# Kernel tuning notes

Hardware: AMD Instinct MI355X
Metric: run time of the kernel (lower is better)

Reference implementation:

```python
import jax, jax.numpy as jnp
import numpy as np

B, N, D, H = 8, 512, 512, 8
DK = D // H          # 64
DIM_G = 64           # trigonometric geometry embedding dim
WAVE_LEN = 1000.0


def box_relational_embedding(f_g):
    # f_g: [B, N, 4] -> [B, N, N, 64]
    x_min, y_min, x_max, y_max = [f_g[..., i] for i in range(4)]  # [B,N]
    cx = (x_min + x_max) * 0.5
    cy = (y_min + y_max) * 0.5
    w = x_max - x_min + 1.0
    h = y_max - y_min + 1.0
    # pairwise deltas; divide by w_i / h_i of the row box (broadcast over j)
    dx = jnp.log(jnp.clip(jnp.abs((cx[:, :, None] - cx[:, None, :]) / w[:, :, None]), 0.001))
    dy = jnp.log(jnp.clip(jnp.abs((cy[:, :, None] - cy[:, None, :]) / h[:, :, None]), 0.001))
    dw = jnp.log(w[:, :, None] / w[:, None, :])
    dh = jnp.log(h[:, :, None] / h[:, None, :])
    pos = jnp.stack([dx, dy, dw, dh], axis=-1)  # [B,N,N,4]
    feat_range = jnp.arange(DIM_G // 8, dtype=jnp.float32) / (DIM_G / 8.0)  # [8]
    dim_mat = 1.0 / (WAVE_LEN ** feat_range)  # [8]
    mul = (100.0 * pos)[..., None] * dim_mat  # [B,N,N,4,8]
    mul = mul.reshape(pos.shape[0], pos.shape[1], pos.shape[2], -1)  # [B,N,N,32]
    return jnp.concatenate([jnp.sin(mul), jnp.cos(mul)], axis=-1)  # [B,N,N,64]


def setup_inputs() -> dict:
    key = jax.random.key(0)
    ks = jax.random.split(key, 12)
    s = 1.0 / np.sqrt(D)
    return {
        "input_query": jax.random.normal(ks[0], (B, N, D), jnp.float32),
        "input_key": jax.random.normal(ks[1], (B, N, D), jnp.float32),
        "input_value": jax.random.normal(ks[2], (B, N, D), jnp.float32),
        "input_box": jax.random.uniform(ks[3], (B, N, 4), jnp.float32),
        "mask": jax.random.randint(ks[4], (B, N), 0, 2, jnp.int32),
        "not_objects": jax.random.randint(ks[5], (B, N), 0, 2).astype(jnp.bool_),
        "Wq": jax.random.normal(ks[6], (D, D), jnp.float32) * s,
        "bq": jnp.zeros((D,), jnp.float32),
        "Wk": jax.random.normal(ks[7], (D, D), jnp.float32) * s,
        "bk": jnp.zeros((D,), jnp.float32),
        "Wv": jax.random.normal(ks[8], (D, D), jnp.float32) * s,
        "bv": jnp.zeros((D,), jnp.float32),
        "Wo": jax.random.normal(ks[9], (D, D), jnp.float32) * s,
        "bo": jnp.zeros((D,), jnp.float32),
        "WG": jax.random.normal(ks[10], (H, DIM_G), jnp.float32) * 0.1,
        "bG": jnp.zeros((H,), jnp.float32),
    }


def reference(input_query, input_key, input_value, input_box, mask, not_objects,
              Wq, bq, Wk, bk, Wv, bv, Wo, bo, WG, bG):
    emb = box_relational_embedding(input_box)  # [B,N,N,64]

    def proj(x, W, b):
        return (x @ W + b).reshape(B, N, H, DK).transpose(0, 2, 1, 3)  # [B,H,N,DK]

    q = proj(input_query, Wq, bq)
    k = proj(input_key, Wk, bk)
    v = proj(input_value, Wv, bv)

    scores = jnp.einsum('bhnd,bhmd->bhnm', q, k) / np.sqrt(DK).astype(np.float32)
    scores = jnp.where(mask[:, None, None, :] == 0, -1e9, scores)

    # per-head geometry weights: [B,H,N,N]
    wg = jax.nn.relu(jnp.einsum('bnmg,hg->bhnm', emb, WG) + bG[None, :, None, None])

    # object mask: zero the geometry log-bias where either i or j is not an object
    pair_not_obj = not_objects[:, None, :, None] | not_objects[:, None, None, :]  # [B,1,N,N]
    mask_obj = 1.0 - pair_not_obj.astype(jnp.float32)

    logits = jnp.log(jnp.clip(wg, 1e-6)) * mask_obj + scores
    attn = jax.nn.softmax(logits, axis=-1)  # dropout is identity in eval mode

    out = jnp.einsum('bhnm,bhmd->bhnd', attn, v)
    out = out.transpose(0, 2, 1, 3).reshape(B, N, D)
    return out @ Wo + bo
```

## Files before the change

### kernel.cpp

```cpp
#include <hip/hip_runtime.h>
#include <hip/hip_fp16.h>

#define B_ 8
#define N_ 512
#define D_ 512
#define H_ 8
#define DK_ 64

typedef unsigned int uint;
typedef unsigned short ushort;
typedef __attribute__((ext_vector_type(8))) short short8;
typedef __attribute__((ext_vector_type(8))) _Float16 half8;
typedef __attribute__((ext_vector_type(4))) float floatx4;

__device__ __forceinline__ float bf2f(ushort s) { return __uint_as_float(((uint)s) << 16); }
__device__ __forceinline__ ushort f2bf(float f) {
    uint x = __float_as_uint(f);
    return (ushort)((x + 0x7fffu + ((x >> 16) & 1u)) >> 16);
}
__device__ __forceinline__ float blo(uint u) { return __uint_as_float(u << 16); }
__device__ __forceinline__ float bhi(uint u) { return __uint_as_float(u & 0xffff0000u); }
__device__ __forceinline__ float ldf(const void* p, size_t i, int isbf) {
    return isbf ? bf2f(((const ushort*)p)[i]) : ((const float*)p)[i];
}
__device__ __forceinline__ short ldb(const void* p, size_t i, int isbf) {
    return isbf ? (short)(((const ushort*)p)[i]) : (short)f2bf(((const float*)p)[i]);
}

__global__ __launch_bounds__(256) void probe_dtype(const uint* __restrict__ q,
                                                   int* __restrict__ flag) {
    __shared__ int s[256];
    const int t = threadIdx.x;
    int cnt = 0;
    for (int i = t; i < 4096; i += 256) {
        const uint e = (q[i] >> 7) & 0xffu;
        cnt += (e >= 0x70u && e <= 0x84u) ? 1 : 0;
    }
    s[t] = cnt;
    __syncthreads();
    for (int d = 128; d > 0; d >>= 1) {
        if (t < d) s[t] += s[t + d];
        __syncthreads();
    }
    if (t == 0) *flag = (s[0] > 3276) ? 1 : 0;
}

__global__ __launch_bounds__(256) void prep_bias(const void* __restrict__ b0,
                                                 const void* __restrict__ b1,
                                                 const void* __restrict__ b2,
                                                 const void* __restrict__ b3,
                                                 float* __restrict__ biasf,
                                                 const int* __restrict__ flagp) {
    const int isbf = *flagp;
    const int e = blockIdx.x * 256 + threadIdx.x;
    const int z = e >> 9;
    const void* src = (z == 0) ? b0 : (z == 1) ? b1 : (z == 2) ? b2 : b3;
    biasf[e] = ldf(src, e & 511, isbf);
}

__global__ __launch_bounds__(256) void transw(const void* __restrict__ w0,
                                              const void* __restrict__ w1,
                                              const void* __restrict__ w2,
                                              const void* __restrict__ w3,
                                              ushort* __restrict__ wt,
                                              const int* __restrict__ flagp) {
    const int isbf = *flagp;
    const int z = blockIdx.z;
    const void* W = (z == 0) ? w0 : (z == 1) ? w1 : (z == 2) ? w2 : w3;
    const int n0 = blockIdx.x * 32, k0 = blockIdx.y * 32;
    __shared__ float tile[32][33];
    const int tx = threadIdx.x & 31, ty = threadIdx.x >> 5;
#pragma unroll
    for (int r = 0; r < 4; ++r)
        tile[ty + 8 * r][tx] = ldf(W, (size_t)(k0 + ty + 8 * r) * D_ + n0 + tx, isbf);
    __syncthreads();
#pragma unroll
    for (int r = 0; r < 4; ++r)
        wt[(size_t)z * 262144 + (size_t)(n0 + ty + 8 * r) * D_ + k0 + tx] =
            f2bf(tile[tx][ty + 8 * r]);
}

template <typename AT, int MODE>
__global__ __launch_bounds__(256) void gemm_mfma(
    const AT* __restrict__ A0, const AT* __restrict__ A1, const AT* __restrict__ A2,
    const ushort* __restrict__ wt, const float* __restrict__ biasf,
    ushort* __restrict__ oq, ushort* __restrict__ ok, ushort* __restrict__ ov,
    void* __restrict__ dout, const int* __restrict__ flagp, int want) {
    if (want >= 0 && *flagp != want) return;
    const int z = (MODE == 0) ? blockIdx.z : 3;
    const AT* A = (MODE == 0) ? ((z == 0) ? A0 : (z == 1) ? A1 : A2) : A0;
    const ushort* W = wt + (size_t)z * 262144;
    const float* bias = biasf + z * 512;
    const int row0 = blockIdx.x * 128, col0 = blockIdx.y * 64;
    const int t = threadIdx.x, wv = t >> 6, lane = t & 63;
    const int m16 = lane & 15, quad = lane >> 4;

    __shared__ ushort As[128][40];
    __shared__ ushort Ws[64][40];
    floatx4 acc[2][4] = {};

    const int ar = t >> 1, ah = t & 1;
    const int wr = t >> 2, wc = (t & 3) * 8;

    for (int k0 = 0; k0 < D_; k0 += 32) {
        __syncthreads();
        {
            const AT* ap = A + (size_t)(row0 + ar) * D_ + k0 + ah * 16;
            short8 s0, s1;
            if constexpr (sizeof(AT) == 4) {
                const float4 f0 = *(const float4*)(ap);
                const float4 f1 = *(const float4*)(ap + 4);
                const float4 f2 = *(const float4*)(ap + 8);
                const float4 f3 = *(const float4*)(ap + 12);
                s0[0] = (short)f2bf(f0.x); s0[1] = (short)f2bf(f0.y);
                s0[2] = (short)f2bf(f0.z); s0[3] = (short)f2bf(f0.w);
                s0[4] = (short)f2bf(f1.x); s0[5] = (short)f2bf(f1.y);
                s0[6] = (short)f2bf(f1.z); s0[7] = (short)f2bf(f1.w);
                s1[0] = (short)f2bf(f2.x); s1[1] = (short)f2bf(f2.y);
                s1[2] = (short)f2bf(f2.z); s1[3] = (short)f2bf(f2.w);
                s1[4] = (short)f2bf(f3.x); s1[5] = (short)f2bf(f3.y);
                s1[6] = (short)f2bf(f3.z); s1[7] = (short)f2bf(f3.w);
            } else {
                s0 = *(const short8*)(ap);
                s1 = *(const short8*)(ap + 8);
            }
            *(short8*)&As[ar][ah * 16] = s0;
            *(short8*)&As[ar][ah * 16 + 8] = s1;
        }
        *(short8*)&Ws[wr][wc] =
            *(const short8*)(W + (size_t)(col0 + wr) * D_ + k0 + wc);
        __syncthreads();

        const short8 a0 = *(const short8*)&As[wv * 32 + m16][quad * 8];
        const short8 a1 = *(const short8*)&As[wv * 32 + 16 + m16][quad * 8];
        const short8 b0 = *(const short8*)&Ws[m16][quad * 8];
        const short8 b1 = *(const short8*)&Ws[16 + m16][quad * 8];
        const short8 b2 = *(const short8*)&Ws[32 + m16][quad * 8];
        const short8 b3 = *(const short8*)&Ws[48 + m16][quad * 8];
        acc[0][0] = __builtin_amdgcn_mfma_f32_16x16x32_bf16(a0, b0, acc[0][0], 0, 0, 0);
        acc[0][1] = __builtin_amdgcn_mfma_f32_16x16x32_bf16(a0, b1, acc[0][1], 0, 0, 0);
        acc[0][2] = __builtin_amdgcn_mfma_f32_16x16x32_bf16(a0, b2, acc[0][2], 0, 0, 0);
        acc[0][3] = __builtin_amdgcn_mfma_f32_16x16x32_bf16(a0, b3, acc[0][3], 0, 0, 0);
        acc[1][0] = __builtin_amdgcn_mfma_f32_16x16x32_bf16(a1, b0, acc[1][0], 0, 0, 0);
        acc[1][1] = __builtin_amdgcn_mfma_f32_16x16x32_bf16(a1, b1, acc[1][1], 0, 0, 0);
        acc[1][2] = __builtin_amdgcn_mfma_f32_16x16x32_bf16(a1, b2, acc[1][2], 0, 0, 0);
        acc[1][3] = __builtin_amdgcn_mfma_f32_16x16x32_bf16(a1, b3, acc[1][3], 0, 0, 0);
    }

    const int isbf = *flagp;
#pragma unroll
    for (int mt = 0; mt < 2; ++mt) {
#pragma unroll
        for (int nt = 0; nt < 4; ++nt) {
            const int colg = col0 + nt * 16 + m16;
            const float bi = bias[colg];
            float v0 = acc[mt][nt][0] + bi, v1 = acc[mt][nt][1] + bi;
            float v2 = acc[mt][nt][2] + bi, v3 = acc[mt][nt][3] + bi;
            const int rowb = row0 + wv * 32 + mt * 16 + quad * 4;
            if (MODE == 0) {
                if (z == 2) {
                    const int bhv = (rowb >> 9) * H_ + (colg >> 6);
                    uint2 pk;
                    pk.x = (uint)f2bf(v0) | ((uint)f2bf(v1) << 16);
                    pk.y = (uint)f2bf(v2) | ((uint)f2bf(v3) << 16);
                    *(uint2*)(ov + ((size_t)bhv * DK_ + (colg & 63)) * N_ + (rowb & 511)) = pk;
                } else {
                    ushort* o = (z == 0) ? oq : ok;
                    const float vv[4] = {v0, v1, v2, v3};
#pragma unroll
                    for (int r = 0; r < 4; ++r) {
                        const int row = rowb + r;
                        o[((size_t)((row >> 9) * H_ + (colg >> 6)) * N_ + (row & 511)) * DK_ +
                          (colg & 63)] = f2bf(vv[r]);
                    }
                }
            } else {
                const float vv[4] = {v0, v1, v2, v3};
#pragma unroll
                for (int r = 0; r < 4; ++r) {
                    const int row = rowb + r;
                    if (isbf) ((ushort*)dout)[(size_t)row * D_ + colg] = f2bf(vv[r]);
                    else      ((float*)dout)[(size_t)row * D_ + colg] = vv[r];
                }
            }
        }
    }
}

__global__ __launch_bounds__(256) void geom2(const void* __restrict__ box,
                                             const int* __restrict__ nobj,
                                             const void* __restrict__ WG,
                                             const void* __restrict__ bG,
                                             ushort* __restrict__ glog,
                                             const int* __restrict__ flagp) {
    const int isbf = *flagp;
    const int i = blockIdx.x, bl = blockIdx.y;
    const int t = threadIdx.x;

    __shared__ _Float16 trig[128][72];
    __shared__ _Float16 wgf[16][72];
    __shared__ float mobja[128];
    __shared__ float bgs[8];

    for (int e = t; e < 1024; e += 256) {
        const int h = e >> 6, g = e & 63;
        wgf[h][g] = (_Float16)((h < 8) ? ldf(WG, (size_t)h * 64 + g, isbf) : 0.f);
    }
    if (t < 8) bgs[t] = ldf(bG, t, isbf);

    const size_t ib = (size_t)(bl * N_ + i) * 4;
    const float ixn = ldf(box, ib + 0, isbf), iyn = ldf(box, ib + 1, isbf);
    const float ixx = ldf(box, ib + 2, isbf), iyx = ldf(box, ib + 3, isbf);
    const float wi = ixx - ixn + 1.0f, hi = iyx - iyn + 1.0f;
    const float cxi = (ixn + ixx) * 0.5f, cyi = (iyn + iyx) * 0.5f;
    const float rwi = 1.0f / wi, rhi = 1.0f / hi;
    const float lwi = __logf(wi), lhi = __logf(hi);
    const int noi = nobj[bl * N_ + i];
    __syncthreads();

    const int wv = t >> 6, lane = t & 63, m16 = lane & 15, quad = lane >> 4;
    const half8 bf0 = *(const half8*)&wgf[m16][quad * 8];
    const half8 bf1 = *(const half8*)&wgf[m16][quad * 8 + 32];
    _Float16* gb = (_Float16*)glog +
                   ((((size_t)bl * 32 + (i >> 4)) * 8) * 16 + (i & 15)) * 512;
    const float dm[8] = {1.0f, 0.421696503f, 0.177827941f, 0.074989421f,
                         0.031622777f, 0.013335214f, 0.005623413f, 0.002371374f};

    for (int c = 0; c < 4; ++c) {
        const int jbase = c * 128;
        {
            const int pair = t >> 1, hf = t & 1;
            const int j = jbase + pair;
            const size_t jb = (size_t)(bl * N_ + j) * 4;
            const float jxn = ldf(box, jb + 0, isbf), jyn = ldf(box, jb + 1, isbf);
            const float jxx = ldf(box, jb + 2, isbf), jyx = ldf(box, jb + 3, isbf);
            const float wj = jxx - jxn + 1.0f, hj = jyx - jyn + 1.0f;
            float p0, p1;
            if (hf == 0) {
                const float cxj = (jxn + jxx) * 0.5f, cyj = (jyn + jyx) * 0.5f;
                p0 = __logf(fmaxf(fabsf((cxi - cxj) * rwi), 0.001f));
                p1 = __logf(fmaxf(fabsf((cyi - cyj) * rhi), 0.001f));
                mobja[pair] = (noi || nobj[bl * N_ + j]) ? 0.f : 1.f;
            } else {
                p0 = lwi - __logf(wj);
                p1 = lhi - __logf(hj);
            }
#pragma unroll
            for (int pp = 0; pp < 2; ++pp) {
                const float base = 100.f * (pp ? p1 : p0);
                half8 s8, c8;
#pragma unroll
                for (int f = 0; f < 8; ++f) {
                    float sv, cv;
                    __sincosf(base * dm[f], &sv, &cv);
                    s8[f] = (_Float16)sv;
                    c8[f] = (_Float16)cv;
                }
                const int g0 = hf * 16 + pp * 8;
                *(half8*)&trig[pair][g0] = s8;
                *(half8*)&trig[pair][32 + g0] = c8;
            }
        }
        __syncthreads();
        {
#pragma unroll
            for (int sub = 0; sub < 2; ++sub) {
                const int pr0 = wv * 32 + sub * 16;
                const half8 a0 = *(const half8*)&trig[pr0 + m16][quad * 8];
                const half8 a1 = *(const half8*)&trig[pr0 + m16][quad * 8 + 32];
                floatx4 acc = {};
                acc = __builtin_amdgcn_mfma_f32_16x16x32_f16(a0, bf0, acc, 0, 0, 0);
                acc = __builtin_amdgcn_mfma_f32_16x16x32_f16(a1, bf1, acc, 0, 0, 0);
                if (m16 < 8) {
#pragma unroll
                    for (int r = 0; r < 4; ++r) {
                        const int pair = pr0 + quad * 4 + r;
                        const float wg = acc[r] + bgs[m16];
                        const float gl = __logf(fmaxf(wg, 1e-6f)) * mobja[pair];
                        gb[(size_t)m16 * 8192 + jbase + pair] = (_Float16)gl;
                    }
                }
            }
        }
        __syncthreads();
    }
}

__global__ __launch_bounds__(256) void attn3(
    const ushort* __restrict__ qw, const ushort* __restrict__ kw,
    const ushort* __restrict__ vt, const int* __restrict__ mask,
    const ushort* __restrict__ glog, ushort* __restrict__ att, int b0) {
    const int it = blockIdx.x, h = blockIdx.y, bl = blockIdx.z;
    const int bg = b0 + bl;
    const int i0 = it * 16;
    const int t = threadIdx.x, wv = t >> 6, lane = t & 63;
    const int m16 = lane & 15, quad = lane >> 4;
    const size_t bh = (size_t)(bg * H_ + h);

    __shared__ float lg[16][516];
    __shared__ ushort sbuf[16 * 520];
    __shared__ float rsumInv[16];

    {
        const uint4* src = (const uint4*)(glog + (((size_t)bl * 32 + it) * 8 + h) * 8192);
        uint4* dst = (uint4*)sbuf;
#pragma unroll
        for (int e = 0; e < 4; ++e) dst[t + 256 * e] = src[t + 256 * e];
    }
    const ushort* qrow = qw + (bh * N_ + i0 + m16) * DK_ + quad * 8;
    const short8 aq0 = *(const short8*)(qrow);
    const short8 aq1 = *(const short8*)(qrow + 32);
    __syncthreads();

#pragma unroll
    for (int tt = 0; tt < 8; ++tt) {
        const int j0 = wv * 128 + tt * 16;
        const ushort* krow = kw + (bh * N_ + j0 + m16) * DK_ + quad * 8;
        const short8 bk0 = *(const short8*)(krow);
        const short8 bk1 = *(const short8*)(krow + 32);
        floatx4 acc = {};
        acc = __builtin_amdgcn_mfma_f32_16x16x32_bf16(aq0, bk0, acc, 0, 0, 0);
        acc = __builtin_amdgcn_mfma_f32_16x16x32_bf16(aq1, bk1, acc, 0, 0, 0);
        const int mj = mask[bg * N_ + j0 + m16];
        const __half* gt = (const __half*)sbuf;
#pragma unroll
        for (int r = 0; r < 4; ++r) {
            const int i = quad * 4 + r;
            const float g = __half2float(gt[i * 512 + j0 + m16]);
            lg[i][j0 + m16] = (mj ? 0.125f * acc[r] : -1e9f) + g;
        }
    }
    __syncthreads();

    {
        const int row = t >> 4, l = t & 15;
        float v[32];
        float mx = -3e38f;
#pragma unroll
        for (int s = 0; s < 32; ++s) { v[s] = lg[row][l + 16 * s]; mx = fmaxf(mx, v[s]); }
#pragma unroll
        for (int d = 1; d < 16; d <<= 1) mx = fmaxf(mx, __shfl_xor(mx, d, 16));
        float sm = 0.f;
#pragma unroll
        for (int s = 0; s < 32; ++s) { const float p = __expf(v[s] - mx); sm += p; v[s] = p; }
#pragma unroll
        for (int d = 1; d < 16; d <<= 1) sm += __shfl_xor(sm, d, 16);
#pragma unroll
        for (int s = 0; s < 32; ++s) sbuf[row * 520 + l + 16 * s] = f2bf(v[s]);
        if (l == 0) rsumInv[row] = 1.0f / sm;
    }
    __syncthreads();

    {
        const int dk0 = wv * 16;
        const ushort* vrow = vt + (bh * DK_ + dk0 + m16) * N_ + quad * 8;
        floatx4 oc = {};
#pragma unroll
        for (int kc = 0; kc < 16; ++kc) {
            const short8 ap = *(const short8*)(sbuf + m16 * 520 + kc * 32 + quad * 8);
            const short8 bv = *(const short8*)(vrow + kc * 32);
            oc = __builtin_amdgcn_mfma_f32_16x16x32_bf16(ap, bv, oc, 0, 0, 0);
        }
#pragma unroll
        for (int r = 0; r < 4; ++r) {
            const int i = quad * 4 + r;
            const float o = oc[r] * rsumInv[i];
            att[((size_t)(bg * N_ + i0 + i)) * D_ + h * DK_ + dk0 + m16] = f2bf(o);
        }
    }
}

__global__ __launch_bounds__(256) void gemm16(const void* __restrict__ A,
                                              const void* __restrict__ W,
                                              const void* __restrict__ bias,
                                              void* __restrict__ out,
                                              const int* __restrict__ flagp,
                                              int a_follows, int mode) {
    const int isbf = *flagp;
    const int a_isbf = a_follows ? isbf : 1;
    const int wave = threadIdx.x >> 6;
    const int tile = blockIdx.x * 4 + wave;
    const int tm = tile >> 5, tn = tile & 31;
    const int row0 = tm * 16, col0 = tn * 16;
    const int lane = threadIdx.x & 63;
    const int m = lane & 15, quad = lane >> 4;
    floatx4 acc = {0.f, 0.f, 0.f, 0.f};
    const size_t abase = (size_t)(row0 + m) * D_ + quad * 8;
    const size_t wbase = (size_t)(quad * 8) * D_ + col0 + m;
    for (int k0 = 0; k0 < D_; k0 += 32) {
        short8 af, bf;
#pragma unroll
        for (int j = 0; j < 8; ++j) af[j] = ldb(A, abase + k0 + j, a_isbf);
#pragma unroll
        for (int j = 0; j < 8; ++j) bf[j] = ldb(W, wbase + (size_t)(k0 + j) * D_, isbf);
        acc = __builtin_amdgcn_mfma_f32_16x16x32_bf16(af, bf, acc, 0, 0, 0);
    }
    const int col = col0 + m;
    const float bi = ldf(bias, col, isbf);
#pragma unroll
    for (int r = 0; r < 4; ++r) {
        const int row = row0 + quad * 4 + r;
        const float v = acc[r] + bi;
        if (mode == 1) {
            ((ushort*)out)[(size_t)(((row >> 9) * H_ + (col >> 6)) * N_ + (row & 511)) * DK_ + (col & 63)] = f2bf(v);
        } else if (isbf) {
            ((ushort*)out)[(size_t)row * D_ + col] = f2bf(v);
        } else {
            ((float*)out)[(size_t)row * D_ + col] = v;
        }
    }
}

__global__ __launch_bounds__(256) void attn_old(
    const ushort* __restrict__ qw, const ushort* __restrict__ kw,
    const ushort* __restrict__ vw, const void* __restrict__ box,
    const int* __restrict__ mask, const int* __restrict__ nobj,
    const void* __restrict__ WG, const void* __restrict__ bG,
    ushort* __restrict__ att, const int* __restrict__ flagp) {
    const int isbf = *flagp;
    const int b = blockIdx.z, h = blockIdx.y;
    const int i0 = blockIdx.x * 8;
    const int t = threadIdx.x;
    __shared__ float lg[8][520];
    __shared__ float q_s[8][68];
    __shared__ float wgh[64];
    __shared__ float cxi[8], cyi[8], rwi[8], rhi[8], lwi[8], lhi[8];
    __shared__ int noi[8];
    __shared__ float rsum[8];
    for (int e = t; e < 512; e += 256) {
        const int ii = e >> 6, dk = e & 63;
        q_s[ii][dk] = bf2f(qw[(size_t)((b * H_ + h) * N_ + i0 + ii) * DK_ + dk]) * 0.125f;
    }
    if (t < 64) wgh[t] = ldf(WG, h * 64 + t, isbf);
    if (t < 8) {
        const size_t bb = (size_t)(b * N_ + i0 + t) * 4;
        const float xmn = ldf(box, bb + 0, isbf), ymn = ldf(box, bb + 1, isbf);
        const float xmx = ldf(box, bb + 2, isbf), ymx = ldf(box, bb + 3, isbf);
        const float w = xmx - xmn + 1.0f, hh = ymx - ymn + 1.0f;
        cxi[t] = (xmn + xmx) * 0.5f;
        cyi[t] = (ymn + ymx) * 0.5f;
        rwi[t] = 1.0f / w;
        rhi[t] = 1.0f / hh;
        lwi[t] = __logf(w);
        lhi[t] = __logf(hh);
        noi[t] = nobj[b * N_ + i0 + t];
    }
    const float bg = ldf(bG, h, isbf);
    __syncthreads();
    for (int jl = 0; jl < 2; ++jl) {
        const int j = t + jl * 256;
        float acc[8];
#pragma unroll
        for (int ii = 0; ii < 8; ++ii) acc[ii] = 0.f;
        const uint4* krow = (const uint4*)(kw + (size_t)((b * H_ + h) * N_ + j) * DK_);
#pragma unroll
        for (int c = 0; c < 8; ++c) {
            const uint4 ku = krow[c];
            float kf[8];
            kf[0] = blo(ku.x); kf[1] = bhi(ku.x); kf[2] = blo(ku.y); kf[3] = bhi(ku.y);
            kf[4] = blo(ku.z); kf[5] = bhi(ku.z); kf[6] = blo(ku.w); kf[7] = bhi(ku.w);
#pragma unroll
            for (int ii = 0; ii < 8; ++ii) {
                const float4 qa = *(const float4*)(&q_s[ii][c * 8]);
                const float4 qb = *(const float4*)(&q_s[ii][c * 8 + 4]);
                acc[ii] += qa.x * kf[0] + qa.y * kf[1] + qa.z * kf[2] + qa.w * kf[3] +
                           qb.x * kf[4] + qb.y * kf[5] + qb.z * kf[6] + qb.w * kf[7];
            }
        }
        const int mj = mask[b * N_ + j];
        const size_t bb = (size_t)(b * N_ + j) * 4;
        const float xmn = ldf(box, bb + 0, isbf), ymn = ldf(box, bb + 1, isbf);
        const float xmx = ldf(box, bb + 2, isbf), ymx = ldf(box, bb + 3, isbf);
        const float cxj = (xmn + xmx) * 0.5f, cyj = (ymn + ymx) * 0.5f;
        const float wj = xmx - xmn + 1.0f, hj = ymx - ymn + 1.0f;
        const float lwj = __logf(wj), lhj = __logf(hj);
        const int noj = nobj[b * N_ + j];
        const float dm[8] = {1.0f, 0.421696503f, 0.177827941f, 0.074989421f,
                             0.031622777f, 0.013335214f, 0.005623413f, 0.002371374f};
        for (int ii = 0; ii < 8; ++ii) {
            const float mobj = (noi[ii] || noj) ? 0.f : 1.f;
            const float dx = __logf(fmaxf(fabsf((cxi[ii] - cxj) * rwi[ii]), 0.001f));
            const float dy = __logf(fmaxf(fabsf((cyi[ii] - cyj) * rhi[ii]), 0.001f));
            const float pos[4] = {dx, dy, lwi[ii] - lwj, lhi[ii] - lhj};
            float wg = bg;
            for (int p = 0; p < 4; ++p) {
                const float base = 100.f * pos[p];
#pragma unroll
                for (int f = 0; f < 8; ++f) {
                    float sv, cv;
                    __sincosf(base * dm[f], &sv, &cv);
                    const int g = p * 8 + f;
                    wg += sv * wgh[g] + cv * wgh[32 + g];
                }
            }
            lg[ii][j] = (mj ? acc[ii] : -1e9f) + __logf(fmaxf(wg, 1e-6f)) * mobj;
        }
    }
    __syncthreads();
    {
        const int rr = t >> 5, l32 = t & 31;
        float mx = -3e38f;
        for (int j = l32; j < N_; j += 32) mx = fmaxf(mx, lg[rr][j]);
#pragma unroll
        for (int d = 1; d < 32; d <<= 1) mx = fmaxf(mx, __shfl_xor(mx, d, 32));
        float sm = 0.f;
        for (int j = l32; j < N_; j += 32) {
            const float p = __expf(lg[rr][j] - mx);
            lg[rr][j] = p;
            sm += p;
        }
#pragma unroll
        for (int d = 1; d < 32; d <<= 1) sm += __shfl_xor(sm, d, 32);
        if (l32 == 0) rsum[rr] = sm;
    }
    __syncthreads();
    {
        const int ii = t >> 5, dkp = t & 31;
        float o0 = 0.f, o1 = 0.f;
        const uint* vbase = (const uint*)vw + (size_t)((b * H_ + h) * N_) * (DK_ / 2) + dkp;
        for (int j = 0; j < N_; ++j) {
            const uint u = vbase[(size_t)j * (DK_ / 2)];
            const float p = lg[ii][j];
            o0 += p * blo(u);
            o1 += p * bhi(u);
        }
        const float inv = 1.0f / rsum[ii];
        const uint pk = (uint)f2bf(o0 * inv) | ((uint)f2bf(o1 * inv) << 16);
        ((uint*)att)[(size_t)(b * N_ + i0 + ii) * (D_ / 2) + h * 32 + dkp] = pk;
    }
}

extern "C" void kernel_launch(void* const* d_in, const int* in_sizes, int n_in,
                              void* d_out, int out_size, void* d_ws, size_t ws_size,
                              hipStream_t stream) {
    const void* xq = d_in[0];
    const void* xk = d_in[1];
    const void* xv = d_in[2];
    const void* box = d_in[3];
    const int* mask = (const int*)d_in[4];
    const int* nobj = (const int*)d_in[5];
    const void* Wq = d_in[6];
    const void* bq = d_in[7];
    const void* Wk = d_in[8];
    const void* bk = d_in[9];
    const void* Wv = d_in[10];
    const void* bv = d_in[11];
    const void* Wo = d_in[12];
    const void* bo = d_in[13];
    const void* WG = d_in[14];
    const void* bG = d_in[15];

    char* ws = (char*)d_ws;
    const size_t MB = 1u << 20;

    if (ws_size >= 54 * MB) {
        int* flag = (int*)ws;
        float* biasf = (float*)(ws + 4096);
        ushort* wt = (ushort*)(ws + 16384);
        size_t p = 16384 + 2097152;
        ushort* qw = (ushort*)(ws + p); p += 4194304;
        ushort* kw = (ushort*)(ws + p); p += 4194304;
        ushort* vt = (ushort*)(ws + p); p += 4194304;
        ushort* att = (ushort*)(ws + p); p += 4194304;
        ushort* glog = (ushort*)(ws + p);

        hipLaunchKernelGGL(probe_dtype, dim3(1), dim3(256), 0, stream, (const uint*)xq, flag);
        hipLaunchKernelGGL(prep_bias, dim3(8), dim3(256), 0, stream, bq, bk, bv, bo, biasf, flag);
        hipLaunchKernelGGL(transw, dim3(16, 16, 4), dim3(256), 0, stream, Wq, Wk, Wv, Wo, wt, flag);
        hipLaunchKernelGGL((gemm_mfma<float, 0>), dim3(32, 8, 3), dim3(256), 0, stream,
                           (const float*)xq, (const float*)xk, (const float*)xv,
                           wt, biasf, qw, kw, vt, (void*)nullptr, flag, 0);
        hipLaunchKernelGGL((gemm_mfma<ushort, 0>), dim3(32, 8, 3), dim3(256), 0, stream,
                           (const ushort*)xq, (const ushort*)xk, (const ushort*)xv,
                           wt, biasf, qw, kw, vt, (void*)nullptr, flag, 1);
        hipLaunchKernelGGL(geom2, dim3(N_, B_), dim3(256), 0, stream,
                           box, nobj, WG, bG, glog, flag);
        hipLaunchKernelGGL(attn3, dim3(32, H_, B_), dim3(256), 0, stream,
                           qw, kw, vt, mask, glog, att, 0);
        hipLaunchKernelGGL((gemm_mfma<ushort, 1>), dim3(32, 8), dim3(256), 0, stream,
                           att, att, att, wt, biasf, qw, kw, vt, d_out, flag, -1);
    } else {
        int* flag = (int*)ws;
        ushort* qw = (ushort*)(ws + 256);
        ushort* kw = (ushort*)(ws + 256 + 4194304);
        ushort* vw = (ushort*)(ws + 256 + 8388608);
        ushort* att = (ushort*)(ws + 256 + 12582912);
        hipLaunchKernelGGL(probe_dtype, dim3(1), dim3(256), 0, stream, (const uint*)xq, flag);
        hipLaunchKernelGGL(gemm16, dim3(2048), dim3(256), 0, stream, xq, Wq, bq, (void*)qw, flag, 1, 1);
        hipLaunchKernelGGL(gemm16, dim3(2048), dim3(256), 0, stream, xk, Wk, bk, (void*)kw, flag, 1, 1);
        hipLaunchKernelGGL(gemm16, dim3(2048), dim3(256), 0, stream, xv, Wv, bv, (void*)vw, flag, 1, 1);
        hipLaunchKernelGGL(attn_old, dim3(N_ / 8, H_, B_), dim3(256), 0, stream,
                           qw, kw, vw, box, mask, nobj, WG, bG, att, flag);
        hipLaunchKernelGGL(gemm16, dim3(2048), dim3(256), 0, stream, att, Wo, bo, d_out, flag, 0, 2);
    }
}
```

Before: 218.4 us.

## Merge bias prep into transpose, unify projection GEMMs, prefetch tiles, vectorize box loads

Folds the bias-conversion kernel into the weight transpose kernel. Replaces the two dtype-specialized QKV GEMM launches with one kernel that branches on the runtime flag, which removes an early-exit launch. Adds register prefetch of the next K tile in both GEMMs so global loads overlap the MFMA work. Also vectorizes the box loads in the geometry kernel and pads its trig shared-memory tile with 4-halfword accesses to reduce bank conflicts. Risks: the runtime dtype branch inside the GEMM and the extra prefetch registers.

```diff
diff --git a/kernel.cpp b/kernel.cpp
--- a/kernel.cpp
+++ b/kernel.cpp
@@ -11,6 +11,7 @@
 typedef unsigned short ushort;
 typedef __attribute__((ext_vector_type(8))) short short8;
 typedef __attribute__((ext_vector_type(8))) _Float16 half8;
+typedef __attribute__((ext_vector_type(4))) _Float16 half4;
 typedef __attribute__((ext_vector_type(4))) float floatx4;
 
 __device__ __forceinline__ float bf2f(ushort s) { return __uint_as_float(((uint)s) << 16); }
@@ -25,6 +26,13 @@
 }
 __device__ __forceinline__ short ldb(const void* p, size_t i, int isbf) {
     return isbf ? (short)(((const ushort*)p)[i]) : (short)f2bf(((const float*)p)[i]);
+}
+__device__ __forceinline__ float4 ldbox(const void* p, size_t row, int isbf) {
+    if (isbf) {
+        const uint2 u = ((const uint2*)p)[row];
+        return make_float4(blo(u.x), bhi(u.x), blo(u.y), bhi(u.y));
+    }
+    return ((const float4*)p)[row];
 }
 
 __global__ __launch_bounds__(256) void probe_dtype(const uint* __restrict__ q,
@@ -45,24 +53,16 @@
     if (t == 0) *flag = (s[0] > 3276) ? 1 : 0;
 }
 
-__global__ __launch_bounds__(256) void prep_bias(const void* __restrict__ b0,
-                                                 const void* __restrict__ b1,
-                                                 const void* __restrict__ b2,
-                                                 const void* __restrict__ b3,
-                                                 float* __restrict__ biasf,
-                                                 const int* __restrict__ flagp) {
-    const int isbf = *flagp;
-    const int e = blockIdx.x * 256 + threadIdx.x;
-    const int z = e >> 9;
-    const void* src = (z == 0) ? b0 : (z == 1) ? b1 : (z == 2) ? b2 : b3;
-    biasf[e] = ldf(src, e & 511, isbf);
-}
-
 __global__ __launch_bounds__(256) void transw(const void* __restrict__ w0,
                                               const void* __restrict__ w1,
                                               const void* __restrict__ w2,
                                               const void* __restrict__ w3,
+                                              const void* __restrict__ b0,
+                                              const void* __restrict__ b1,
+                                              const void* __restrict__ b2,
+                                              const void* __restrict__ b3,
                                               ushort* __restrict__ wt,
+                                              float* __restrict__ biasf,
                                               const int* __restrict__ flagp) {
     const int isbf = *flagp;
     const int z = blockIdx.z;
@@ -73,6 +73,11 @@
 #pragma unroll
     for (int r = 0; r < 4; ++r)
         tile[ty + 8 * r][tx] = ldf(W, (size_t)(k0 + ty + 8 * r) * D_ + n0 + tx, isbf);
+    if (blockIdx.x == 0 && blockIdx.y == 0) {
+        const void* bz = (z == 0) ? b0 : (z == 1) ? b1 : (z == 2) ? b2 : b3;
+        for (int e = threadIdx.x; e < 512; e += 256)
+            biasf[z * 512 + e] = ldf(bz, e, isbf);
+    }
     __syncthreads();
 #pragma unroll
     for (int r = 0; r < 4; ++r)
@@ -80,15 +85,14 @@
             f2bf(tile[tx][ty + 8 * r]);
 }
 
-template <typename AT, int MODE>
-__global__ __launch_bounds__(256) void gemm_mfma(
-    const AT* __restrict__ A0, const AT* __restrict__ A1, const AT* __restrict__ A2,
+__global__ __launch_bounds__(256) void gemm0(
+    const void* __restrict__ A0, const void* __restrict__ A1, const void* __restrict__ A2,
     const ushort* __restrict__ wt, const float* __restrict__ biasf,
     ushort* __restrict__ oq, ushort* __restrict__ ok, ushort* __restrict__ ov,
-    void* __restrict__ dout, const int* __restrict__ flagp, int want) {
-    if (want >= 0 && *flagp != want) return;
-    const int z = (MODE == 0) ? blockIdx.z : 3;
-    const AT* A = (MODE == 0) ? ((z == 0) ? A0 : (z == 1) ? A1 : A2) : A0;
+    const int* __restrict__ flagp) {
+    const int isbf = *flagp;
+    const int z = blockIdx.z;
+    const char* A = (const char*)((z == 0) ? A0 : (z == 1) ? A1 : A2);
     const ushort* W = wt + (size_t)z * 262144;
     const float* bias = biasf + z * 512;
     const int row0 = blockIdx.x * 128, col0 = blockIdx.y * 64;
@@ -102,34 +106,48 @@
     const int ar = t >> 1, ah = t & 1;
     const int wr = t >> 2, wc = (t & 3) * 8;
 
+    float4 pf0, pf1, pf2, pf3;
+    short8 ps0, ps1, pw;
+
+    auto loadA = [&](int k0) {
+        const size_t e = (size_t)(row0 + ar) * D_ + k0 + ah * 16;
+        if (isbf) {
+            ps0 = *(const short8*)(A + 2 * e);
+            ps1 = *(const short8*)(A + 2 * e + 16);
+        } else {
+            const float* ap = (const float*)(A + 4 * e);
+            pf0 = *(const float4*)(ap);
+            pf1 = *(const float4*)(ap + 4);
+            pf2 = *(const float4*)(ap + 8);
+            pf3 = *(const float4*)(ap + 12);
+        }
+        pw = *(const short8*)(W + (size_t)(col0 + wr) * D_ + k0 + wc);
+    };
+    auto stage = [&]() {
+        short8 s0, s1;
+        if (isbf) {
+            s0 = ps0; s1 = ps1;
+        } else {
+            s0[0] = (short)f2bf(pf0.x); s0[1] = (short)f2bf(pf0.y);
+            s0[2] = (short)f2bf(pf0.z); s0[3] = (short)f2bf(pf0.w);
+            s0[4] = (short)f2bf(pf1.x); s0[5] = (short)f2bf(pf1.y);
+            s0[6] = (short)f2bf(pf1.z); s0[7] = (short)f2bf(pf1.w);
+            s1[0] = (short)f2bf(pf2.x); s1[1] = (short)f2bf(pf2.y);
+            s1[2] = (short)f2bf(pf2.z); s1[3] = (short)f2bf(pf2.w);
+            s1[4] = (short)f2bf(pf3.x); s1[5] = (short)f2bf(pf3.y);
+            s1[6] = (short)f2bf(pf3.z); s1[7] = (short)f2bf(pf3.w);
+        }
+        *(short8*)&As[ar][ah * 16] = s0;
+        *(short8*)&As[ar][ah * 16 + 8] = s1;
+        *(short8*)&Ws[wr][wc] = pw;
+    };
+
+    loadA(0);
     for (int k0 = 0; k0 < D_; k0 += 32) {
         __syncthreads();
-        {
-            const AT* ap = A + (size_t)(row0 + ar) * D_ + k0 + ah * 16;
-            short8 s0, s1;
-            if constexpr (sizeof(AT) == 4) {
-                const float4 f0 = *(const float4*)(ap);
-                const float4 f1 = *(const float4*)(ap + 4);
-                const float4 f2 = *(const float4*)(ap + 8);
-                const float4 f3 = *(const float4*)(ap + 12);
-                s0[0] = (short)f2bf(f0.x); s0[1] = (short)f2bf(f0.y);
-                s0[2] = (short)f2bf(f0.z); s0[3] = (short)f2bf(f0.w);
-                s0[4] = (short)f2bf(f1.x); s0[5] = (short)f2bf(f1.y);
-                s0[6] = (short)f2bf(f1.z); s0[7] = (short)f2bf(f1.w);
-                s1[0] = (short)f2bf(f2.x); s1[1] = (short)f2bf(f2.y);
-                s1[2] = (short)f2bf(f2.z); s1[3] = (short)f2bf(f2.w);
-                s1[4] = (short)f2bf(f3.x); s1[5] = (short)f2bf(f3.y);
-                s1[6] = (short)f2bf(f3.z); s1[7] = (short)f2bf(f3.w);
-            } else {
-                s0 = *(const short8*)(ap);
-                s1 = *(const short8*)(ap + 8);
-            }
-            *(short8*)&As[ar][ah * 16] = s0;
-            *(short8*)&As[ar][ah * 16 + 8] = s1;
-        }
-        *(short8*)&Ws[wr][wc] =
-            *(const short8*)(W + (size_t)(col0 + wr) * D_ + k0 + wc);
+        stage();
         __syncthreads();
+        if (k0 + 32 < D_) loadA(k0 + 32);
 
         const short8 a0 = *(const short8*)&As[wv * 32 + m16][quad * 8];
         const short8 a1 = *(const short8*)&As[wv * 32 + 16 + m16][quad * 8];
@@ -147,41 +165,98 @@
         acc[1][3] = __builtin_amdgcn_mfma_f32_16x16x32_bf16(a1, b3, acc[1][3], 0, 0, 0);
     }
 
-    const int isbf = *flagp;
 #pragma unroll
     for (int mt = 0; mt < 2; ++mt) {
 #pragma unroll
         for (int nt = 0; nt < 4; ++nt) {
             const int colg = col0 + nt * 16 + m16;
             const float bi = bias[colg];
-            float v0 = acc[mt][nt][0] + bi, v1 = acc[mt][nt][1] + bi;
-            float v2 = acc[mt][nt][2] + bi, v3 = acc[mt][nt][3] + bi;
+            const float v0 = acc[mt][nt][0] + bi, v1 = acc[mt][nt][1] + bi;
+            const float v2 = acc[mt][nt][2] + bi, v3 = acc[mt][nt][3] + bi;
             const int rowb = row0 + wv * 32 + mt * 16 + quad * 4;
-            if (MODE == 0) {
-                if (z == 2) {
-                    const int bhv = (rowb >> 9) * H_ + (colg >> 6);
-                    uint2 pk;
-                    pk.x = (uint)f2bf(v0) | ((uint)f2bf(v1) << 16);
-                    pk.y = (uint)f2bf(v2) | ((uint)f2bf(v3) << 16);
-                    *(uint2*)(ov + ((size_t)bhv * DK_ + (colg & 63)) * N_ + (rowb & 511)) = pk;
-                } else {
-                    ushort* o = (z == 0) ? oq : ok;
-                    const float vv[4] = {v0, v1, v2, v3};
-#pragma unroll
-                    for (int r = 0; r < 4; ++r) {
-                        const int row = rowb + r;
-                        o[((size_t)((row >> 9) * H_ + (colg >> 6)) * N_ + (row & 511)) * DK_ +
-                          (colg & 63)] = f2bf(vv[r]);
-                    }
-                }
+            if (z == 2) {
+                const int bhv = (rowb >> 9) * H_ + (colg >> 6);
+                uint2 pk;
+                pk.x = (uint)f2bf(v0) | ((uint)f2bf(v1) << 16);
+                pk.y = (uint)f2bf(v2) | ((uint)f2bf(v3) << 16);
+                *(uint2*)(ov + ((size_t)bhv * DK_ + (colg & 63)) * N_ + (rowb & 511)) = pk;
             } else {
+                ushort* o = (z == 0) ? oq : ok;
                 const float vv[4] = {v0, v1, v2, v3};
 #pragma unroll
                 for (int r = 0; r < 4; ++r) {
                     const int row = rowb + r;
-                    if (isbf) ((ushort*)dout)[(size_t)row * D_ + colg] = f2bf(vv[r]);
-                    else      ((float*)dout)[(size_t)row * D_ + colg] = vv[r];
+                    o[((size_t)((row >> 9) * H_ + (colg >> 6)) * N_ + (row & 511)) * DK_ +
+                      (colg & 63)] = f2bf(vv[r]);
                 }
+            }
+        }
+    }
+}
+
+__global__ __launch_bounds__(256) void gemm1(
+    const ushort* __restrict__ att, const ushort* __restrict__ wt,
+    const float* __restrict__ biasf, void* __restrict__ dout,
+    const int* __restrict__ flagp) {
+    const int isbf = *flagp;
+    const ushort* W = wt + (size_t)3 * 262144;
+    const float* bias = biasf + 3 * 512;
+    const int row0 = blockIdx.x * 128, col0 = blockIdx.y * 64;
+    const int t = threadIdx.x, wv = t >> 6, lane = t & 63;
+    const int m16 = lane & 15, quad = lane >> 4;
+
+    __shared__ ushort As[128][40];
+    __shared__ ushort Ws[64][40];
+    floatx4 acc[2][4] = {};
+
+    const int ar = t >> 1, ah = t & 1;
+    const int wr = t >> 2, wc = (t & 3) * 8;
+
+    short8 ps0, ps1, pw;
+    auto loadA = [&](int k0) {
+        const ushort* ap = att + (size_t)(row0 + ar) * D_ + k0 + ah * 16;
+        ps0 = *(const short8*)(ap);
+        ps1 = *(const short8*)(ap + 8);
+        pw = *(const short8*)(W + (size_t)(col0 + wr) * D_ + k0 + wc);
+    };
+
+    loadA(0);
+    for (int k0 = 0; k0 < D_; k0 += 32) {
+        __syncthreads();
+        *(short8*)&As[ar][ah * 16] = ps0;
+        *(short8*)&As[ar][ah * 16 + 8] = ps1;
+        *(short8*)&Ws[wr][wc] = pw;
+        __syncthreads();
+        if (k0 + 32 < D_) loadA(k0 + 32);
+
+        const short8 a0 = *(const short8*)&As[wv * 32 + m16][quad * 8];
+        const short8 a1 = *(const short8*)&As[wv * 32 + 16 + m16][quad * 8];
+        const short8 b0 = *(const short8*)&Ws[m16][quad * 8];
+        const short8 b1 = *(const short8*)&Ws[16 + m16][quad * 8];
+        const short8 b2 = *(const short8*)&Ws[32 + m16][quad * 8];
+        const short8 b3 = *(const short8*)&Ws[48 + m16][quad * 8];
+        acc[0][0] = __builtin_amdgcn_mfma_f32_16x16x32_bf16(a0, b0, acc[0][0], 0, 0, 0);
+        acc[0][1] = __builtin_amdgcn_mfma_f32_16x16x32_bf16(a0, b1, acc[0][1], 0, 0, 0);
+        acc[0][2] = __builtin_amdgcn_mfma_f32_16x16x32_bf16(a0, b2, acc[0][2], 0, 0, 0);
+        acc[0][3] = __builtin_amdgcn_mfma_f32_16x16x32_bf16(a0, b3, acc[0][3], 0, 0, 0);
+        acc[1][0] = __builtin_amdgcn_mfma_f32_16x16x32_bf16(a1, b0, acc[1][0], 0, 0, 0);
+        acc[1][1] = __builtin_amdgcn_mfma_f32_16x16x32_bf16(a1, b1, acc[1][1], 0, 0, 0);
+        acc[1][2] = __builtin_amdgcn_mfma_f32_16x16x32_bf16(a1, b2, acc[1][2], 0, 0, 0);
+        acc[1][3] = __builtin_amdgcn_mfma_f32_16x16x32_bf16(a1, b3, acc[1][3], 0, 0, 0);
+    }
+
+#pragma unroll
+    for (int mt = 0; mt < 2; ++mt) {
+#pragma unroll
+        for (int nt = 0; nt < 4; ++nt) {
+            const int colg = col0 + nt * 16 + m16;
+            const float bi = bias[colg];
+#pragma unroll
+            for (int r = 0; r < 4; ++r) {
+                const int row = row0 + wv * 32 + mt * 16 + quad * 4 + r;
+                const float v = acc[mt][nt][r] + bi;
+                if (isbf) ((ushort*)dout)[(size_t)row * D_ + colg] = f2bf(v);
+                else      ((float*)dout)[(size_t)row * D_ + colg] = v;
             }
         }
     }
@@ -197,7 +272,7 @@
     const int i = blockIdx.x, bl = blockIdx.y;
     const int t = threadIdx.x;
 
-    __shared__ _Float16 trig[128][72];
+    __shared__ _Float16 trig[128][76];
     __shared__ _Float16 wgf[16][72];
     __shared__ float mobja[128];
     __shared__ float bgs[8];
@@ -208,11 +283,9 @@
     }
     if (t < 8) bgs[t] = ldf(bG, t, isbf);
 
-    const size_t ib = (size_t)(bl * N_ + i) * 4;
-    const float ixn = ldf(box, ib + 0, isbf), iyn = ldf(box, ib + 1, isbf);
-    const float ixx = ldf(box, ib + 2, isbf), iyx = ldf(box, ib + 3, isbf);
-    const float wi = ixx - ixn + 1.0f, hi = iyx - iyn + 1.0f;
-    const float cxi = (ixn + ixx) * 0.5f, cyi = (iyn + iyx) * 0.5f;
+    const float4 bi4 = ldbox(box, (size_t)bl * N_ + i, isbf);
+    const float wi = bi4.z - bi4.x + 1.0f, hi = bi4.w - bi4.y + 1.0f;
+    const float cxi = (bi4.x + bi4.z) * 0.5f, cyi = (bi4.y + bi4.w) * 0.5f;
     const float rwi = 1.0f / wi, rhi = 1.0f / hi;
     const float lwi = __logf(wi), lhi = __logf(hi);
     const int noi = nobj[bl * N_ + i];
@@ -231,13 +304,11 @@
         {
             const int pair = t >> 1, hf = t & 1;
             const int j = jbase + pair;
-            const size_t jb = (size_t)(bl * N_ + j) * 4;
-            const float jxn = ldf(box, jb + 0, isbf), jyn = ldf(box, jb + 1, isbf);
-            const float jxx = ldf(box, jb + 2, isbf), jyx = ldf(box, jb + 3, isbf);
-            const float wj = jxx - jxn + 1.0f, hj = jyx - jyn + 1.0f;
+            const float4 bj4 = ldbox(box, (size_t)bl * N_ + j, isbf);
+            const float wj = bj4.z - bj4.x + 1.0f, hj = bj4.w - bj4.y + 1.0f;
             float p0, p1;
             if (hf == 0) {
-                const float cxj = (jxn + jxx) * 0.5f, cyj = (jyn + jyx) * 0.5f;
+                const float cxj = (bj4.x + bj4.z) * 0.5f, cyj = (bj4.y + bj4.w) * 0.5f;
                 p0 = __logf(fmaxf(fabsf((cxi - cxj) * rwi), 0.001f));
                 p1 = __logf(fmaxf(fabsf((cyi - cyj) * rhi), 0.001f));
                 mobja[pair] = (noi || nobj[bl * N_ + j]) ? 0.f : 1.f;
@@ -257,24 +328,29 @@
                     c8[f] = (_Float16)cv;
                 }
                 const int g0 = hf * 16 + pp * 8;
-                *(half8*)&trig[pair][g0] = s8;
-                *(half8*)&trig[pair][32 + g0] = c8;
+                *(half4*)&trig[pair][g0]          = *(const half4*)&s8;
+                *(half4*)&trig[pair][g0 + 4]      = *((const half4*)&s8 + 1);
+                *(half4*)&trig[pair][32 + g0]     = *(const half4*)&c8;
+                *(half4*)&trig[pair][32 + g0 + 4] = *((const half4*)&c8 + 1);
             }
         }
         __syncthreads();
         {
 #pragma unroll
             for (int sub = 0; sub < 2; ++sub) {
-                const int pr0 = wv * 32 + sub * 16;
-                const half8 a0 = *(const half8*)&trig[pr0 + m16][quad * 8];
-                const half8 a1 = *(const half8*)&trig[pr0 + m16][quad * 8 + 32];
+                const int row = wv * 32 + sub * 16 + m16;
+                half8 a0, a1;
+                *((half4*)&a0)     = *(const half4*)&trig[row][quad * 8];
+                *((half4*)&a0 + 1) = *(const half4*)&trig[row][quad * 8 + 4];
+                *((half4*)&a1)     = *(const half4*)&trig[row][32 + quad * 8];
+                *((half4*)&a1 + 1) = *(const half4*)&trig[row][32 + quad * 8 + 4];
                 floatx4 acc = {};
                 acc = __builtin_amdgcn_mfma_f32_16x16x32_f16(a0, bf0, acc, 0, 0, 0);
                 acc = __builtin_amdgcn_mfma_f32_16x16x32_f16(a1, bf1, acc, 0, 0, 0);
                 if (m16 < 8) {
 #pragma unroll
                     for (int r = 0; r < 4; ++r) {
-                        const int pair = pr0 + quad * 4 + r;
+                        const int pair = wv * 32 + sub * 16 + quad * 4 + r;
                         const float wg = acc[r] + bgs[m16];
                         const float gl = __logf(fmaxf(wg, 1e-6f)) * mobja[pair];
                         gb[(size_t)m16 * 8192 + jbase + pair] = (_Float16)gl;
@@ -565,20 +641,16 @@
         ushort* glog = (ushort*)(ws + p);
 
         hipLaunchKernelGGL(probe_dtype, dim3(1), dim3(256), 0, stream, (const uint*)xq, flag);
-        hipLaunchKernelGGL(prep_bias, dim3(8), dim3(256), 0, stream, bq, bk, bv, bo, biasf, flag);
-        hipLaunchKernelGGL(transw, dim3(16, 16, 4), dim3(256), 0, stream, Wq, Wk, Wv, Wo, wt, flag);
-        hipLaunchKernelGGL((gemm_mfma<float, 0>), dim3(32, 8, 3), dim3(256), 0, stream,
-                           (const float*)xq, (const float*)xk, (const float*)xv,
-                           wt, biasf, qw, kw, vt, (void*)nullptr, flag, 0);
-        hipLaunchKernelGGL((gemm_mfma<ushort, 0>), dim3(32, 8, 3), dim3(256), 0, stream,
-                           (const ushort*)xq, (const ushort*)xk, (const ushort*)xv,
-                           wt, biasf, qw, kw, vt, (void*)nullptr, flag, 1);
+        hipLaunchKernelGGL(transw, dim3(16, 16, 4), dim3(256), 0, stream,
+                           Wq, Wk, Wv, Wo, bq, bk, bv, bo, wt, biasf, flag);
+        hipLaunchKernelGGL(gemm0, dim3(32, 8, 3), dim3(256), 0, stream,
+                           xq, xk, xv, wt, biasf, qw, kw, vt, flag);
         hipLaunchKernelGGL(geom2, dim3(N_, B_), dim3(256), 0, stream,
                            box, nobj, WG, bG, glog, flag);
         hipLaunchKernelGGL(attn3, dim3(32, H_, B_), dim3(256), 0, stream,
                            qw, kw, vt, mask, glog, att, 0);
-        hipLaunchKernelGGL((gemm_mfma<ushort, 1>), dim3(32, 8), dim3(256), 0, stream,
-                           att, att, att, wt, biasf, qw, kw, vt, d_out, flag, -1);
+        hipLaunchKernelGGL(gemm1, dim3(32, 8), dim3(256), 0, stream,
+                           att, wt, biasf, d_out, flag);
     } else {
         int* flag = (int*)ws;
         ushort* qw = (ushort*)(ws + 256);
```

After: 210.1 us. 1.04x faster.
